# Kernel optimization log

Hardware: AMD Instinct MI355X
Metric: run time of the kernel (lower is better)

The kernel has to match this reference:

```python
import jax, jax.numpy as jnp
import numpy as np

DIM = 256
N = 8192

def setup_inputs() -> dict:
    key = jax.random.key(0)
    kx, kq, kk, kv = jax.random.split(key, 4)
    X = jax.random.normal(kx, (N, DIM), dtype=jnp.float32)
    # nn.Linear weights are [out, in]; xavier-uniform-like scale via normal/sqrt(dim)
    Wq = jax.random.normal(kq, (DIM, DIM), dtype=jnp.float32) / np.sqrt(DIM)
    Wk = jax.random.normal(kk, (DIM, DIM), dtype=jnp.float32) / np.sqrt(DIM)
    Wv = jax.random.normal(kv, (DIM, DIM), dtype=jnp.float32) / np.sqrt(DIM)
    return {"X": X, "Wq": Wq, "Wk": Wk, "Wv": Wv}

def reference(X, Wq, Wk, Wv):
    # nn.Linear(no bias): y = X @ W.T
    Q = X @ Wq.T  # [N, D]
    K = X @ Wk.T
    V = X @ Wv.T
    scores = (Q @ K.T) / jnp.sqrt(jnp.asarray(DIM, dtype=X.dtype))  # [N, N]
    softed = jax.nn.softmax(scores, axis=-1)
    return softed @ V  # [N, D]
```

## Files before the change

### kernel.cpp

```cpp
#include <hip/hip_runtime.h>
#include <math.h>

#define N 8192
#define D 256
#define QBLK 128
#define KBLK 64

typedef float f32x4 __attribute__((ext_vector_type(4)));
typedef short bf16x8 __attribute__((ext_vector_type(8)));

#define MFMA(a, b, c) __builtin_amdgcn_mfma_f32_16x16x32_bf16((a), (b), (c), 0, 0, 0)

__device__ __forceinline__ unsigned short f2b(float f) {
    unsigned u = __builtin_bit_cast(unsigned, f);
    u = u + 0x7fffu + ((u >> 16) & 1u);
    return (unsigned short)(u >> 16);
}
__device__ __forceinline__ unsigned pk2(float a, float b) {
    return (unsigned)f2b(a) | ((unsigned)f2b(b) << 16);
}
__device__ __forceinline__ float b2f(short s) {
    unsigned x = ((unsigned)(unsigned short)s) << 16;
    return __builtin_bit_cast(float, x);
}

__global__ __launch_bounds__(256) void proj_mfma(
    const float* __restrict__ X, const float* __restrict__ Wq,
    const float* __restrict__ Wk, const float* __restrict__ Wv,
    unsigned short* __restrict__ Qb, unsigned short* __restrict__ Kb,
    unsigned short* __restrict__ Vt)
{
    __shared__ char Wl[32768];
    const int z = blockIdx.z;
    const float* W = (z == 0) ? Wq : (z == 1) ? Wk : Wv;
    const int r0 = blockIdx.x * 64;
    const int c0 = blockIdx.y * 64;
    const int t = threadIdx.x, w = t >> 6, l = t & 63;
    const int lo = l & 15, hi = l >> 4;

    #pragma unroll
    for (int i = 0; i < 16; ++i) {
        int e4 = t + i * 256;
        int col = e4 >> 6, kk4 = e4 & 63;
        float4 f = *(const float4*)&W[(size_t)(c0 + col) * D + kk4 * 4];
        unsigned long long v = (unsigned long long)pk2(f.x, f.y)
                             | ((unsigned long long)pk2(f.z, f.w) << 32);
        *(unsigned long long*)(Wl + col * 512 + ((kk4 * 8) ^ ((col & 7) << 4))) = v;
    }
    __syncthreads();

    bf16x8 xf[8];
    {
        const float* xr = X + (size_t)(r0 + w * 16 + lo) * D;
        #pragma unroll
        for (int ks = 0; ks < 8; ++ks) {
            float4 a = *(const float4*)(xr + ks * 32 + hi * 8);
            float4 b = *(const float4*)(xr + ks * 32 + hi * 8 + 4);
            bf16x8 v;
            v[0] = (short)f2b(a.x); v[1] = (short)f2b(a.y);
            v[2] = (short)f2b(a.z); v[3] = (short)f2b(a.w);
            v[4] = (short)f2b(b.x); v[5] = (short)f2b(b.y);
            v[6] = (short)f2b(b.z); v[7] = (short)f2b(b.w);
            xf[ks] = v;
        }
    }

    f32x4 acc[4];
    #pragma unroll
    for (int nc = 0; nc < 4; ++nc) acc[nc] = (f32x4){0.f, 0.f, 0.f, 0.f};
    #pragma unroll
    for (int ks = 0; ks < 8; ++ks) {
        #pragma unroll
        for (int nc = 0; nc < 4; ++nc) {
            int col = nc * 16 + lo;
            bf16x8 wf = *(const bf16x8*)(Wl + col * 512 +
                                         ((ks * 64 + hi * 16) ^ ((col & 7) << 4)));
            acc[nc] = MFMA(xf[ks], wf, acc[nc]);
        }
    }

    if (z < 2) {
        unsigned short* Y = z ? Kb : Qb;
        #pragma unroll
        for (int nc = 0; nc < 4; ++nc)
            #pragma unroll
            for (int r = 0; r < 4; ++r)
                Y[(size_t)(r0 + w * 16 + hi * 4 + r) * D + c0 + nc * 16 + lo] = f2b(acc[nc][r]);
    } else {
        #pragma unroll
        for (int nc = 0; nc < 4; ++nc) {
            unsigned long long v = (unsigned long long)pk2(acc[nc][0], acc[nc][1])
                                 | ((unsigned long long)pk2(acc[nc][2], acc[nc][3]) << 32);
            *(unsigned long long*)&Vt[(size_t)(c0 + nc * 16 + lo) * N + r0 + w * 16 + hi * 4] = v;
        }
    }
}

__device__ __forceinline__ void stage_tile(
    const unsigned short* __restrict__ Kb, const unsigned short* __restrict__ Vt,
    char* kbuf, char* vbuf, int kt, int w, int l)
{
    #pragma unroll
    for (int i = 0; i < 8; ++i) {
        int c = w * 8 + i;
        int dst = c * 64 + l;
        {
            int key = dst >> 5, xc = dst & 31;
            const unsigned short* gp = Kb + (size_t)(kt + key) * D + (xc ^ (key & 7)) * 8;
            __builtin_amdgcn_global_load_lds(
                (const __attribute__((address_space(1))) void*)gp,
                (__attribute__((address_space(3))) void*)(kbuf + c * 1024), 16, 0, 0);
        }
        {
            int dd = dst >> 3, xc = dst & 7;
            const unsigned short* gp = Vt + (size_t)dd * N + kt + (xc ^ (dd & 7)) * 8;
            __builtin_amdgcn_global_load_lds(
                (const __attribute__((address_space(1))) void*)gp,
                (__attribute__((address_space(3))) void*)(vbuf + c * 1024), 16, 0, 0);
        }
    }
}

template <int KSPLIT>
__global__ __launch_bounds__(256) void attn_mfma(
    const unsigned short* __restrict__ Qb,
    const unsigned short* __restrict__ Kb,
    const unsigned short* __restrict__ Vt,
    unsigned short* __restrict__ Opart,
    float2* __restrict__ ml)
{
    extern __shared__ char smem[];
    const int t = threadIdx.x;
    const int w = t >> 6;
    const int l = t & 63;
    const int lo = l & 15;
    const int hi = l >> 4;
    const int q0 = blockIdx.x * QBLK + w * 32;
    const int split = blockIdx.y;
    const int kbase = split * (N / KSPLIT);
    const int NTS = N / KSPLIT / KBLK;

    char* Pw = smem + 131072 + w * 4608;

    bf16x8 qf[2][8];
    #pragma unroll
    for (int s = 0; s < 2; ++s) {
        const unsigned short* qrow = Qb + (size_t)(q0 + s * 16 + lo) * D;
        #pragma unroll
        for (int ks = 0; ks < 8; ++ks)
            qf[s][ks] = *(const bf16x8*)(qrow + ks * 32 + hi * 8);
    }

    stage_tile(Kb, Vt, smem, smem + 65536, kbase, w, l);

    f32x4 Oacc[2][16];
    #pragma unroll
    for (int s = 0; s < 2; ++s)
        #pragma unroll
        for (int i = 0; i < 16; ++i) Oacc[s][i] = (f32x4){0.f, 0.f, 0.f, 0.f};
    float m_run[2] = {-INFINITY, -INFINITY};
    float l_run[2] = {0.f, 0.f};
    const float scale = 0.0625f;

    __syncthreads();

    for (int tt = 0; tt < NTS; ++tt) {
        const int cur = tt & 1;
        if (tt + 1 < NTS)
            stage_tile(Kb, Vt, smem + (cur ^ 1) * 32768, smem + 65536 + (cur ^ 1) * 32768,
                       kbase + (tt + 1) * KBLK, w, l);

        const char* Kl = smem + cur * 32768;
        const char* Vl = smem + 65536 + cur * 32768;

        f32x4 sacc[2][4];
        #pragma unroll
        for (int s = 0; s < 2; ++s)
            #pragma unroll
            for (int kg = 0; kg < 4; ++kg) sacc[s][kg] = (f32x4){0.f, 0.f, 0.f, 0.f};
        #pragma unroll
        for (int ks = 0; ks < 8; ++ks) {
            #pragma unroll
            for (int kg = 0; kg < 4; ++kg) {
                int key = kg * 16 + lo;
                bf16x8 kf = *(const bf16x8*)(Kl + key * 512 +
                                             ((ks * 64 + hi * 16) ^ ((key & 7) << 4)));
                sacc[0][kg] = MFMA(kf, qf[0][ks], sacc[0][kg]);
                sacc[1][kg] = MFMA(kf, qf[1][ks], sacc[1][kg]);
            }
        }

        float mx[2];
        #pragma unroll
        for (int s = 0; s < 2; ++s) {
            float m = -INFINITY;
            #pragma unroll
            for (int kg = 0; kg < 4; ++kg)
                #pragma unroll
                for (int r = 0; r < 4; ++r) m = fmaxf(m, sacc[s][kg][r]);
            m *= scale;
            m = fmaxf(m, __shfl_xor(m, 16));
            m = fmaxf(m, __shfl_xor(m, 32));
            mx[s] = m;
        }

        bool need = (mx[0] > m_run[0] + 8.0f) || (mx[1] > m_run[1] + 8.0f);
        if (__any(need)) {
            #pragma unroll
            for (int s = 0; s < 2; ++s) {
                float m_new = fmaxf(m_run[s], mx[s]);
                float corr = __expf(m_run[s] - m_new);
                m_run[s] = m_new;
                l_run[s] *= corr;
                float cr0 = __shfl(corr, hi * 4 + 0);
                float cr1 = __shfl(corr, hi * 4 + 1);
                float cr2 = __shfl(corr, hi * 4 + 2);
                float cr3 = __shfl(corr, hi * 4 + 3);
                #pragma unroll
                for (int nc = 0; nc < 16; ++nc) {
                    Oacc[s][nc][0] *= cr0; Oacc[s][nc][1] *= cr1;
                    Oacc[s][nc][2] *= cr2; Oacc[s][nc][3] *= cr3;
                }
            }
        }

        float p[2][16];
        #pragma unroll
        for (int s = 0; s < 2; ++s) {
            float ts = 0.f;
            #pragma unroll
            for (int kg = 0; kg < 4; ++kg)
                #pragma unroll
                for (int r = 0; r < 4; ++r) {
                    float pv = __expf(sacc[s][kg][r] * scale - m_run[s]);
                    p[s][kg * 4 + r] = pv;
                    ts += pv;
                }
            ts += __shfl_xor(ts, 16);
            ts += __shfl_xor(ts, 32);
            l_run[s] += ts;
        }

        #pragma unroll
        for (int s = 0; s < 2; ++s) {
            char* pr = Pw + (s * 16 + lo) * 144;
            #pragma unroll
            for (int kg = 0; kg < 4; ++kg) {
                *(unsigned*)(pr + (kg * 16 + hi * 4) * 2)     = pk2(p[s][kg * 4 + 0], p[s][kg * 4 + 1]);
                *(unsigned*)(pr + (kg * 16 + hi * 4 + 2) * 2) = pk2(p[s][kg * 4 + 2], p[s][kg * 4 + 3]);
            }
        }
        __threadfence_block();

        bf16x8 pa[2][2];
        #pragma unroll
        for (int s = 0; s < 2; ++s) {
            pa[s][0] = *(const bf16x8*)(Pw + (s * 16 + lo) * 144 + hi * 16);
            pa[s][1] = *(const bf16x8*)(Pw + (s * 16 + lo) * 144 + 64 + hi * 16);
        }

        #pragma unroll
        for (int nc = 0; nc < 16; ++nc) {
            int dd = nc * 16 + lo;
            bf16x8 v0 = *(const bf16x8*)(Vl + dd * 128 + ((hi * 16) ^ ((dd & 7) << 4)));
            bf16x8 v1 = *(const bf16x8*)(Vl + dd * 128 + ((64 + hi * 16) ^ ((dd & 7) << 4)));
            Oacc[0][nc] = MFMA(pa[0][0], v0, Oacc[0][nc]);
            Oacc[0][nc] = MFMA(pa[0][1], v1, Oacc[0][nc]);
            Oacc[1][nc] = MFMA(pa[1][0], v0, Oacc[1][nc]);
            Oacc[1][nc] = MFMA(pa[1][1], v1, Oacc[1][nc]);
        }

        __syncthreads();
    }

    #pragma unroll
    for (int s = 0; s < 2; ++s) {
        const int qrow = q0 + s * 16 + hi * 4;
        #pragma unroll
        for (int nc = 0; nc < 16; ++nc)
            #pragma unroll
            for (int r = 0; r < 4; ++r)
                Opart[((size_t)split * N + qrow + r) * D + nc * 16 + lo] = f2b(Oacc[s][nc][r]);
        if (hi == 0)
            ml[(size_t)split * N + q0 + s * 16 + lo] = make_float2(m_run[s], l_run[s]);
    }
}

__global__ __launch_bounds__(256) void combine_kernel(
    const unsigned short* __restrict__ Opart, const float2* __restrict__ ml,
    float* __restrict__ out, int nsplit)
{
    int idx = blockIdx.x * 256 + threadIdx.x;
    int q = idx >> 5;
    int d0 = (idx & 31) * 8;

    float M = -INFINITY;
    for (int i = 0; i < nsplit; ++i) M = fmaxf(M, ml[(size_t)i * N + q].x);
    float L = 0.f;
    float acc[8] = {};
    for (int i = 0; i < nsplit; ++i) {
        float2 v = ml[(size_t)i * N + q];
        float wgt = __expf(v.x - M);
        L += wgt * v.y;
        bf16x8 ov = *(const bf16x8*)&Opart[((size_t)i * N + q) * D + d0];
        #pragma unroll
        for (int j = 0; j < 8; ++j) acc[j] += wgt * b2f(ov[j]);
    }
    float r = 1.f / L;
    #pragma unroll
    for (int j = 0; j < 8; ++j) out[(size_t)q * D + d0 + j] = acc[j] * r;
}

extern "C" void kernel_launch(void* const* d_in, const int* in_sizes, int n_in,
                              void* d_out, int out_size, void* d_ws, size_t ws_size,
                              hipStream_t stream) {
    const float* X  = (const float*)d_in[0];
    const float* Wq = (const float*)d_in[1];
    const float* Wk = (const float*)d_in[2];
    const float* Wv = (const float*)d_in[3];

    unsigned short* ws = (unsigned short*)d_ws;
    const size_t ndq = (size_t)N * D;
    unsigned short* Qb = ws;
    unsigned short* Kb = ws + ndq;
    unsigned short* Vt = ws + 2 * ndq;
    unsigned short* Opart = ws + 3 * ndq;

    const size_t need4 = 7 * ndq * 2 + (size_t)4 * N * 8;
    const int ksplit = (ws_size >= need4) ? 4 : 2;
    float2* ml = (float2*)(ws + (3 + ksplit) * ndq);

    (void)hipFuncSetAttribute((const void*)attn_mfma<4>,
                              hipFuncAttributeMaxDynamicSharedMemorySize, 149504);
    (void)hipFuncSetAttribute((const void*)attn_mfma<2>,
                              hipFuncAttributeMaxDynamicSharedMemorySize, 149504);

    proj_mfma<<<dim3(N / 64, D / 64, 3), 256, 0, stream>>>(X, Wq, Wk, Wv, Qb, Kb, Vt);
    if (ksplit == 4)
        attn_mfma<4><<<dim3(N / QBLK, 4), 256, 149504, stream>>>(Qb, Kb, Vt, Opart, ml);
    else
        attn_mfma<2><<<dim3(N / QBLK, 2), 256, 149504, stream>>>(Qb, Kb, Vt, Opart, ml);
    combine_kernel<<<(N * D / 8) / 256, 256, 0, stream>>>(Opart, ml, (float*)d_out, ksplit);
}
```

Before: 140.0 us.

## Double query block to 8 waves and keep softmax probabilities in registers

Raises the attention block to 256 queries with 512 threads, so each staged K/V tile is reused by twice as many waves. K rows are permuted at staging time so the score-MFMA output layout matches the P operand layout. This removes the per-wave LDS round-trip for P and uses the hardware packed bf16 convert instead of software rounding. It also adds MFMA priority hints and an 8-way key split when the workspace allows it. The costs are higher register pressure, fewer blocks resident per CU, and more partial outputs for the combine kernel to merge.

```diff
diff --git a/kernel.cpp b/kernel.cpp
--- a/kernel.cpp
+++ b/kernel.cpp
@@ -3,7 +3,7 @@
 
 #define N 8192
 #define D 256
-#define QBLK 128
+#define QBLK 256
 #define KBLK 64
 
 typedef float f32x4 __attribute__((ext_vector_type(4)));
@@ -18,6 +18,11 @@
 }
 __device__ __forceinline__ unsigned pk2(float a, float b) {
     return (unsigned)f2b(a) | ((unsigned)f2b(b) << 16);
+}
+__device__ __forceinline__ unsigned cvtpk(float a, float b) {
+    unsigned r;
+    asm("v_cvt_pk_bf16_f32 %0, %1, %2" : "=v"(r) : "v"(a), "v"(b));
+    return r;
 }
 __device__ __forceinline__ float b2f(short s) {
     unsigned x = ((unsigned)(unsigned short)s) << 16;
@@ -96,33 +101,34 @@
     }
 }
 
-__device__ __forceinline__ void stage_tile(
+__device__ __forceinline__ void stage_tile8(
     const unsigned short* __restrict__ Kb, const unsigned short* __restrict__ Vt,
-    char* kbuf, char* vbuf, int kt, int w, int l)
+    char* kbuf, char* vbuf, int kt, int t)
 {
     #pragma unroll
-    for (int i = 0; i < 8; ++i) {
-        int c = w * 8 + i;
-        int dst = c * 64 + l;
+    for (int i = 0; i < 4; ++i) {
+        int c = t + i * 512;
         {
-            int key = dst >> 5, xc = dst & 31;
-            const unsigned short* gp = Kb + (size_t)(kt + key) * D + (xc ^ (key & 7)) * 8;
+            int row = c >> 5, xc = c & 31;
+            int pk = ((row >> 5) << 5) | (((row >> 2) & 3) << 3)
+                   | (((row >> 4) & 1) << 2) | (row & 3);
+            const unsigned short* gp = Kb + (size_t)(kt + pk) * D + (xc ^ (row & 7)) * 8;
             __builtin_amdgcn_global_load_lds(
                 (const __attribute__((address_space(1))) void*)gp,
-                (__attribute__((address_space(3))) void*)(kbuf + c * 1024), 16, 0, 0);
+                (__attribute__((address_space(3))) void*)(kbuf + c * 16), 16, 0, 0);
         }
         {
-            int dd = dst >> 3, xc = dst & 7;
+            int dd = c >> 3, xc = c & 7;
             const unsigned short* gp = Vt + (size_t)dd * N + kt + (xc ^ (dd & 7)) * 8;
             __builtin_amdgcn_global_load_lds(
                 (const __attribute__((address_space(1))) void*)gp,
-                (__attribute__((address_space(3))) void*)(vbuf + c * 1024), 16, 0, 0);
+                (__attribute__((address_space(3))) void*)(vbuf + c * 16), 16, 0, 0);
         }
     }
 }
 
 template <int KSPLIT>
-__global__ __launch_bounds__(256) void attn_mfma(
+__global__ __launch_bounds__(512, 2) void attn_mfma(
     const unsigned short* __restrict__ Qb,
     const unsigned short* __restrict__ Kb,
     const unsigned short* __restrict__ Vt,
@@ -140,8 +146,6 @@
     const int kbase = split * (N / KSPLIT);
     const int NTS = N / KSPLIT / KBLK;
 
-    char* Pw = smem + 131072 + w * 4608;
-
     bf16x8 qf[2][8];
     #pragma unroll
     for (int s = 0; s < 2; ++s) {
@@ -151,7 +155,7 @@
             qf[s][ks] = *(const bf16x8*)(qrow + ks * 32 + hi * 8);
     }
 
-    stage_tile(Kb, Vt, smem, smem + 65536, kbase, w, l);
+    stage_tile8(Kb, Vt, smem, smem + 65536, kbase, t);
 
     f32x4 Oacc[2][16];
     #pragma unroll
@@ -167,8 +171,9 @@
     for (int tt = 0; tt < NTS; ++tt) {
         const int cur = tt & 1;
         if (tt + 1 < NTS)
-            stage_tile(Kb, Vt, smem + (cur ^ 1) * 32768, smem + 65536 + (cur ^ 1) * 32768,
-                       kbase + (tt + 1) * KBLK, w, l);
+            stage_tile8(Kb, Vt, smem + (cur ^ 1) * 32768,
+                        smem + 65536 + (cur ^ 1) * 32768,
+                        kbase + (tt + 1) * KBLK, t);
 
         const char* Kl = smem + cur * 32768;
         const char* Vl = smem + 65536 + cur * 32768;
@@ -178,6 +183,7 @@
         for (int s = 0; s < 2; ++s)
             #pragma unroll
             for (int kg = 0; kg < 4; ++kg) sacc[s][kg] = (f32x4){0.f, 0.f, 0.f, 0.f};
+        __builtin_amdgcn_s_setprio(1);
         #pragma unroll
         for (int ks = 0; ks < 8; ++ks) {
             #pragma unroll
@@ -189,6 +195,7 @@
                 sacc[1][kg] = MFMA(kf, qf[1][ks], sacc[1][kg]);
             }
         }
+        __builtin_amdgcn_s_setprio(0);
 
         float mx[2];
         #pragma unroll
@@ -224,41 +231,34 @@
             }
         }
 
-        float p[2][16];
+        bf16x8 pa[2][2];
         #pragma unroll
         for (int s = 0; s < 2; ++s) {
+            float p[16];
             float ts = 0.f;
             #pragma unroll
             for (int kg = 0; kg < 4; ++kg)
                 #pragma unroll
                 for (int r = 0; r < 4; ++r) {
                     float pv = __expf(sacc[s][kg][r] * scale - m_run[s]);
-                    p[s][kg * 4 + r] = pv;
+                    p[kg * 4 + r] = pv;
                     ts += pv;
                 }
             ts += __shfl_xor(ts, 16);
             ts += __shfl_xor(ts, 32);
             l_run[s] += ts;
-        }
-
-        #pragma unroll
-        for (int s = 0; s < 2; ++s) {
-            char* pr = Pw + (s * 16 + lo) * 144;
-            #pragma unroll
-            for (int kg = 0; kg < 4; ++kg) {
-                *(unsigned*)(pr + (kg * 16 + hi * 4) * 2)     = pk2(p[s][kg * 4 + 0], p[s][kg * 4 + 1]);
-                *(unsigned*)(pr + (kg * 16 + hi * 4 + 2) * 2) = pk2(p[s][kg * 4 + 2], p[s][kg * 4 + 3]);
+
+            union { unsigned u[4]; bf16x8 v; } u0, u1;
+            #pragma unroll
+            for (int j = 0; j < 4; ++j) {
+                u0.u[j] = cvtpk(p[j * 2], p[j * 2 + 1]);
+                u1.u[j] = cvtpk(p[8 + j * 2], p[8 + j * 2 + 1]);
             }
-        }
-        __threadfence_block();
-
-        bf16x8 pa[2][2];
-        #pragma unroll
-        for (int s = 0; s < 2; ++s) {
-            pa[s][0] = *(const bf16x8*)(Pw + (s * 16 + lo) * 144 + hi * 16);
-            pa[s][1] = *(const bf16x8*)(Pw + (s * 16 + lo) * 144 + 64 + hi * 16);
-        }
-
+            pa[s][0] = u0.v;
+            pa[s][1] = u1.v;
+        }
+
+        __builtin_amdgcn_s_setprio(1);
         #pragma unroll
         for (int nc = 0; nc < 16; ++nc) {
             int dd = nc * 16 + lo;
@@ -269,6 +269,7 @@
             Oacc[1][nc] = MFMA(pa[1][0], v0, Oacc[1][nc]);
             Oacc[1][nc] = MFMA(pa[1][1], v1, Oacc[1][nc]);
         }
+        __builtin_amdgcn_s_setprio(0);
 
         __syncthreads();
     }
@@ -326,19 +327,25 @@
     unsigned short* Vt = ws + 2 * ndq;
     unsigned short* Opart = ws + 3 * ndq;
 
-    const size_t need4 = 7 * ndq * 2 + (size_t)4 * N * 8;
-    const int ksplit = (ws_size >= need4) ? 4 : 2;
+    auto need = [ndq](int ks) {
+        return (size_t)(3 + ks) * ndq * 2 + (size_t)ks * N * 8;
+    };
+    const int ksplit = (ws_size >= need(8)) ? 8 : (ws_size >= need(4)) ? 4 : 2;
     float2* ml = (float2*)(ws + (3 + ksplit) * ndq);
 
+    (void)hipFuncSetAttribute((const void*)attn_mfma<8>,
+                              hipFuncAttributeMaxDynamicSharedMemorySize, 131072);
     (void)hipFuncSetAttribute((const void*)attn_mfma<4>,
-                              hipFuncAttributeMaxDynamicSharedMemorySize, 149504);
+                              hipFuncAttributeMaxDynamicSharedMemorySize, 131072);
     (void)hipFuncSetAttribute((const void*)attn_mfma<2>,
-                              hipFuncAttributeMaxDynamicSharedMemorySize, 149504);
+                              hipFuncAttributeMaxDynamicSharedMemorySize, 131072);
 
     proj_mfma<<<dim3(N / 64, D / 64, 3), 256, 0, stream>>>(X, Wq, Wk, Wv, Qb, Kb, Vt);
-    if (ksplit == 4)
-        attn_mfma<4><<<dim3(N / QBLK, 4), 256, 149504, stream>>>(Qb, Kb, Vt, Opart, ml);
+    if (ksplit == 8)
+        attn_mfma<8><<<dim3(N / QBLK, 8), 512, 131072, stream>>>(Qb, Kb, Vt, Opart, ml);
+    else if (ksplit == 4)
+        attn_mfma<4><<<dim3(N / QBLK, 4), 512, 131072, stream>>>(Qb, Kb, Vt, Opart, ml);
     else
-        attn_mfma<2><<<dim3(N / QBLK, 2), 256, 149504, stream>>>(Qb, Kb, Vt, Opart, ml);
+        attn_mfma<2><<<dim3(N / QBLK, 2), 512, 131072, stream>>>(Qb, Kb, Vt, Opart, ml);
     combine_kernel<<<(N * D / 8) / 256, 256, 0, stream>>>(Opart, ml, (float*)d_out, ksplit);
 }
```

After: 128.7 us. -8.1%, faster.
